# Kernel optimization log

Measured on AMD Instinct MI355X. Metric: run time of the kernel, lower is better.

The kernel has to match this reference:

```python
import jax, jax.numpy as jnp
import numpy as np
from math import sqrt

B, L, H, E = 8, 2048, 16, 128
S = 256  # selected_freq_count


def setup_inputs() -> dict:
    key = jax.random.key(0)
    kq, kk, kv = jax.random.split(key, 3)
    rng = np.random.default_rng(0)
    # unique sorted indices in [0, L//2), mirroring get_random_frequencies
    index_q = jnp.asarray(np.sort(rng.choice(L // 2, size=S, replace=False)), dtype=jnp.int32)
    index_kv = jnp.asarray(np.sort(rng.choice(L // 2, size=S, replace=False)), dtype=jnp.int32)
    return {
        "q": jax.random.normal(kq, (B, L, H, E), dtype=jnp.float32),
        "k": jax.random.normal(kk, (B, L, H, E), dtype=jnp.float32),
        "v": jax.random.normal(kv, (B, L, H, E), dtype=jnp.float32),
        "attn_mask": jnp.zeros((1,), dtype=jnp.int32),  # unused by the module
        "index_q": index_q,
        "index_kv": index_kv,
    }


def reference(q, k, v, attn_mask, index_q, index_kv):
    b, l, h, e = q.shape
    scale = 1.0 / sqrt(e)
    # permute to [B, H, E, L] then gather selected frequency columns
    xq = jnp.transpose(q, (0, 2, 3, 1))  # bhel
    xk = jnp.transpose(k, (0, 2, 3, 1))  # bhel
    xq_ft = jnp.take(xq, index_q, axis=-1)   # [B,H,E,Sq]
    xk_ft = jnp.take(xk, index_kv, axis=-1)  # [B,H,E,Sk]
    # dense attention on the gathered subset (contract over E)
    xqk = jax.nn.softmax(scale * jnp.einsum('bhex,bhey->bhxy', xq_ft, xk_ft), axis=-1)
    # NOTE: original multiplies attention by xk_ft_ (v is unused) -- faithful
    xqkv = jnp.einsum('bhxy,bhey->bhex', xqk, xk_ft)  # [B,H,E,Sq]
    # scatter back into zero-initialized [B,H,E,L]
    out_ft = jnp.zeros((b, h, e, l), dtype=q.dtype).at[..., index_q].set(xqkv)
    return out_ft, xqk
```

## Files before the change

### kernel.cpp

```cpp
#include <hip/hip_runtime.h>
#include <math.h>

typedef __bf16 bf16_t;
typedef __attribute__((ext_vector_type(8))) __bf16 bf16x8;
typedef __attribute__((ext_vector_type(4))) float f32x4;

#define NB 8
#define NL 2048
#define NH 16
#define NE 128
#define NS 256
#define XT 64

#define QSTR 136
#define PSTR 72

__global__ __launch_bounds__(256, 3) void fsa_gemm(
    const float* __restrict__ q, const float* __restrict__ k,
    const int* __restrict__ iq, const int* __restrict__ ikv,
    float* __restrict__ out)
{
  float* out_ft = out;
  float* out_p  = out + (size_t)NB*NH*NE*NL;

  __shared__ __align__(16) char smem[34816];
  bf16_t* Qs = (bf16_t*)smem;
  bf16_t* Ks = (bf16_t*)(smem + 17408);
  bf16_t* Ps = (bf16_t*)smem;
  bf16_t* Kt = (bf16_t*)(smem + 9216);

  const int t = threadIdx.x;
  const int tile = (blockIdx.x & 7) * 64 + (blockIdx.x >> 3);
  const int bh = tile >> 2, xb = tile & 3;
  const int b = bh >> 4, h = bh & 15;
  const int x0 = xb * XT;

  const int w   = t >> 6;
  const int l15 = t & 15;
  const int lg  = (t & 63) >> 4;

  {
    const int e4 = t & 31, xr = t >> 5;
    #pragma unroll
    for (int p = 0; p < 8; ++p) {
      const int x  = xr + 8*p;
      const int lq = iq[x0 + x];
      const float4 v = *(const float4*)(q + ((size_t)(b*NL + lq)*NH + h)*NE + 4*e4);
      union { bf16_t h4[4]; uint2 u; } pk;
      pk.h4[0]=(bf16_t)v.x; pk.h4[1]=(bf16_t)v.y; pk.h4[2]=(bf16_t)v.z; pk.h4[3]=(bf16_t)v.w;
      *(uint2*)(Qs + x*QSTR + 4*e4) = pk.u;
    }
  }

  f32x4 acc1[16];
  #pragma unroll
  for (int i = 0; i < 16; ++i) acc1[i] = (f32x4){0.f,0.f,0.f,0.f};
  bf16x8 aQ[4];

  #pragma unroll
  for (int c = 0; c < 4; ++c) {
    if (c > 0) __syncthreads();
    {
      const int e4 = t & 31, yr = t >> 5;
      #pragma unroll
      for (int p = 0; p < 8; ++p) {
        const int y  = yr + 8*p;
        const int lk = ikv[c*64 + y];
        const float4 v = *(const float4*)(k + ((size_t)(b*NL + lk)*NH + h)*NE + 4*e4);
        union { bf16_t h4[4]; uint2 u; } pk;
        pk.h4[0]=(bf16_t)v.x; pk.h4[1]=(bf16_t)v.y; pk.h4[2]=(bf16_t)v.z; pk.h4[3]=(bf16_t)v.w;
        *(uint2*)(Ks + y*QSTR + 4*e4) = pk.u;
      }
    }
    __syncthreads();
    if (c == 0) {
      #pragma unroll
      for (int ks = 0; ks < 4; ++ks)
        aQ[ks] = *(const bf16x8*)(Qs + (w*16 + l15)*QSTR + ks*32 + lg*8);
    }
    #pragma unroll
    for (int ks = 0; ks < 4; ++ks) {
      #pragma unroll
      for (int yt = 0; yt < 4; ++yt) {
        const bf16x8 bk = *(const bf16x8*)(Ks + (yt*16 + l15)*QSTR + ks*32 + lg*8);
        acc1[c*4 + yt] = __builtin_amdgcn_mfma_f32_16x16x32_bf16(aQ[ks], bk, acc1[c*4 + yt], 0, 0, 0);
      }
    }
  }

  const float scale = 0.08838834764831845f;
  #pragma unroll
  for (int r = 0; r < 4; ++r) {
    float m = -3.4e38f;
    #pragma unroll
    for (int yt = 0; yt < 16; ++yt) { acc1[yt][r] *= scale; m = fmaxf(m, acc1[yt][r]); }
    m = fmaxf(m, __shfl_xor(m, 1)); m = fmaxf(m, __shfl_xor(m, 2));
    m = fmaxf(m, __shfl_xor(m, 4)); m = fmaxf(m, __shfl_xor(m, 8));
    float s = 0.f;
    #pragma unroll
    for (int yt = 0; yt < 16; ++yt) { const float e = __expf(acc1[yt][r] - m); acc1[yt][r] = e; s += e; }
    s += __shfl_xor(s, 1); s += __shfl_xor(s, 2); s += __shfl_xor(s, 4); s += __shfl_xor(s, 8);
    const float inv = 1.0f / s;
    #pragma unroll
    for (int yt = 0; yt < 16; ++yt) acc1[yt][r] *= inv;
  }

  {
    float* po = out_p + ((size_t)bh*NS + x0 + w*16 + lg*4)*NS + l15;
    #pragma unroll
    for (int r = 0; r < 4; ++r)
      #pragma unroll
      for (int yt = 0; yt < 16; ++yt)
        po[(size_t)r*NS + yt*16] = acc1[yt][r];
  }

  f32x4 acc2[2][4];
  #pragma unroll
  for (int et = 0; et < 2; ++et)
    #pragma unroll
    for (int xt = 0; xt < 4; ++xt) acc2[et][xt] = (f32x4){0.f,0.f,0.f,0.f};

  #pragma unroll
  for (int c = 0; c < 4; ++c) {
    __syncthreads();
    {
      const int xr = w*16 + lg*4;
      #pragma unroll
      for (int r = 0; r < 4; ++r)
        #pragma unroll
        for (int yt = 0; yt < 4; ++yt)
          Ps[(xr + r)*PSTR + yt*16 + l15] = (bf16_t)acc1[c*4 + yt][r];
    }
    {
      const int e4 = t & 31, yb = t >> 5;
      const int swz = (e4 & 7) << 3;
      #pragma unroll
      for (int p = 0; p < 4; ++p) {
        const int y0  = 2*(yb + 8*p);
        const int ys  = y0 ^ swz;
        const int lk0 = ikv[c*64 + y0];
        const int lk1 = ikv[c*64 + y0 + 1];
        const float4 va = *(const float4*)(k + ((size_t)(b*NL + lk0)*NH + h)*NE + 4*e4);
        const float4 vb = *(const float4*)(k + ((size_t)(b*NL + lk1)*NH + h)*NE + 4*e4);
        union { bf16_t h2[2]; unsigned u; } pr;
        pr.h2[0]=(bf16_t)va.x; pr.h2[1]=(bf16_t)vb.x; *(unsigned*)(Kt + (4*e4+0)*PSTR + ys) = pr.u;
        pr.h2[0]=(bf16_t)va.y; pr.h2[1]=(bf16_t)vb.y; *(unsigned*)(Kt + (4*e4+1)*PSTR + ys) = pr.u;
        pr.h2[0]=(bf16_t)va.z; pr.h2[1]=(bf16_t)vb.z; *(unsigned*)(Kt + (4*e4+2)*PSTR + ys) = pr.u;
        pr.h2[0]=(bf16_t)va.w; pr.h2[1]=(bf16_t)vb.w; *(unsigned*)(Kt + (4*e4+3)*PSTR + ys) = pr.u;
      }
    }
    __syncthreads();
    #pragma unroll
    for (int ks = 0; ks < 2; ++ks) {
      const int er0 = w*32 + l15, er1 = w*32 + 16 + l15;
      const int sw0 = ((er0 >> 2) & 7) << 3;
      const int sw1 = ((er1 >> 2) & 7) << 3;
      const bf16x8 aK0 = *(const bf16x8*)(Kt + er0*PSTR + ((ks*32 + lg*8) ^ sw0));
      const bf16x8 aK1 = *(const bf16x8*)(Kt + er1*PSTR + ((ks*32 + lg*8) ^ sw1));
      #pragma unroll
      for (int xt = 0; xt < 4; ++xt) {
        const bf16x8 bp = *(const bf16x8*)(Ps + (xt*16 + l15)*PSTR + ks*32 + lg*8);
        acc2[0][xt] = __builtin_amdgcn_mfma_f32_16x16x32_bf16(aK0, bp, acc2[0][xt], 0, 0, 0);
        acc2[1][xt] = __builtin_amdgcn_mfma_f32_16x16x32_bf16(aK1, bp, acc2[1][xt], 0, 0, 0);
      }
    }
  }

  #pragma unroll
  for (int et = 0; et < 2; ++et)
    #pragma unroll
    for (int xt = 0; xt < 4; ++xt)
      #pragma unroll
      for (int r = 0; r < 4; ++r) {
        const int e = w*32 + et*16 + lg*4 + r;
        out_ft[((size_t)bh*NE + e)*NL + x0 + xt*16 + l15] = acc2[et][xt][r];
      }
}

__global__ __launch_bounds__(256) void fsa_expand(
    const int* __restrict__ iq, float* __restrict__ out_ft)
{
  __shared__ int   inv[NL];
  __shared__ float oc[16][NS];
  const int t  = threadIdx.x;
  const int bh = blockIdx.x >> 3;
  const int eg = blockIdx.x & 7;

  {
    const int4 mi = {-1,-1,-1,-1};
    *(int4*)(inv + 8*t)     = mi;
    *(int4*)(inv + 8*t + 4) = mi;
  }
  __syncthreads();
  inv[iq[t]] = t;
  {
    const int row = t >> 4, c0 = (t & 15) * 16;
    const float* src = out_ft + ((size_t)bh*NE + eg*16 + row)*NL;
    #pragma unroll
    for (int p = 0; p < 4; ++p)
      *(float4*)&oc[row][c0 + 4*p] = *(const float4*)(src + c0 + 4*p);
  }
  __syncthreads();

  #pragma unroll
  for (int r = 0; r < 16; ++r) {
    float* dst = out_ft + ((size_t)bh*NE + eg*16 + r)*NL;
    #pragma unroll
    for (int half = 0; half < 2; ++half) {
      const int l = half*1024 + 4*t;
      f32x4 v;
      { const int i0 = inv[l+0]; v.x = (i0 >= 0) ? oc[r][i0] : 0.f; }
      { const int i1 = inv[l+1]; v.y = (i1 >= 0) ? oc[r][i1] : 0.f; }
      { const int i2 = inv[l+2]; v.z = (i2 >= 0) ? oc[r][i2] : 0.f; }
      { const int i3 = inv[l+3]; v.w = (i3 >= 0) ? oc[r][i3] : 0.f; }
      __builtin_nontemporal_store(v, (f32x4*)(dst + l));
    }
  }
}

extern "C" void kernel_launch(void* const* d_in, const int* in_sizes, int n_in,
                              void* d_out, int out_size, void* d_ws, size_t ws_size,
                              hipStream_t stream) {
  const float* q = (const float*)d_in[0];
  const float* k = (const float*)d_in[1];
  const int* iq  = (const int*)d_in[4];
  const int* ikv = (const int*)d_in[5];
  float* out = (float*)d_out;

  fsa_gemm<<<dim3(NB*NH*(NS/XT)), dim3(256), 0, stream>>>(q, k, iq, ikv, out);
  fsa_expand<<<dim3(NB*NH*8), dim3(256), 0, stream>>>(iq, out);
}
```

Measured before the change: 358.7 us.

## Fuse scatter-expand into GEMM kernel, writing each tile's output segment directly

Removes the separate expand kernel. Each GEMM block stages its compact output in shared memory, builds a local inverse index over its own L range (between neighbouring selected indices), and writes the scattered rows plus zero-fill directly. The upper half of L (never indexed) is zeroed by blocks split by xb. This avoids the write-then-reread round trip of the compact output through global memory and one launch. In exchange it adds more shared memory per block and scalar tail loops, and it relies on the indices being sorted and below L/2, an assumption that holds for the test inputs.

```diff
diff --git a/kernel.cpp b/kernel.cpp
--- a/kernel.cpp
+++ b/kernel.cpp
@@ -7,6 +7,7 @@
 
 #define NB 8
 #define NL 2048
+#define NLH 1024
 #define NH 16
 #define NE 128
 #define NS 256
@@ -14,6 +15,7 @@
 
 #define QSTR 136
 #define PSTR 72
+#define OSTR 68
 
 __global__ __launch_bounds__(256, 3) void fsa_gemm(
     const float* __restrict__ q, const float* __restrict__ k,
@@ -23,11 +25,13 @@
   float* out_ft = out;
   float* out_p  = out + (size_t)NB*NH*NE*NL;
 
-  __shared__ __align__(16) char smem[34816];
+  __shared__ __align__(16) char smem[38912];
   bf16_t* Qs = (bf16_t*)smem;
   bf16_t* Ks = (bf16_t*)(smem + 17408);
   bf16_t* Ps = (bf16_t*)smem;
   bf16_t* Kt = (bf16_t*)(smem + 9216);
+  float*  Ocomp = (float*)smem;
+  int*    inv   = (int*)(smem + 34816);
 
   const int t = threadIdx.x;
   const int tile = (blockIdx.x & 7) * 64 + (blockIdx.x >> 3);
@@ -100,9 +104,9 @@
     #pragma unroll
     for (int yt = 0; yt < 16; ++yt) { const float e = __expf(acc1[yt][r] - m); acc1[yt][r] = e; s += e; }
     s += __shfl_xor(s, 1); s += __shfl_xor(s, 2); s += __shfl_xor(s, 4); s += __shfl_xor(s, 8);
-    const float inv = 1.0f / s;
-    #pragma unroll
-    for (int yt = 0; yt < 16; ++yt) acc1[yt][r] *= inv;
+    const float inv_ = 1.0f / s;
+    #pragma unroll
+    for (int yt = 0; yt < 16; ++yt) acc1[yt][r] *= inv_;
   }
 
   {
@@ -166,54 +170,48 @@
     }
   }
 
-  #pragma unroll
-  for (int et = 0; et < 2; ++et)
-    #pragma unroll
-    for (int xt = 0; xt < 4; ++xt)
-      #pragma unroll
-      for (int r = 0; r < 4; ++r) {
-        const int e = w*32 + et*16 + lg*4 + r;
-        out_ft[((size_t)bh*NE + e)*NL + x0 + xt*16 + l15] = acc2[et][xt][r];
-      }
-}
-
-__global__ __launch_bounds__(256) void fsa_expand(
-    const int* __restrict__ iq, float* __restrict__ out_ft)
-{
-  __shared__ int   inv[NL];
-  __shared__ float oc[16][NS];
-  const int t  = threadIdx.x;
-  const int bh = blockIdx.x >> 3;
-  const int eg = blockIdx.x & 7;
-
-  {
-    const int4 mi = {-1,-1,-1,-1};
-    *(int4*)(inv + 8*t)     = mi;
-    *(int4*)(inv + 8*t + 4) = mi;
-  }
   __syncthreads();
-  inv[iq[t]] = t;
-  {
-    const int row = t >> 4, c0 = (t & 15) * 16;
-    const float* src = out_ft + ((size_t)bh*NE + eg*16 + row)*NL;
-    #pragma unroll
-    for (int p = 0; p < 4; ++p)
-      *(float4*)&oc[row][c0 + 4*p] = *(const float4*)(src + c0 + 4*p);
-  }
+  {
+    #pragma unroll
+    for (int et = 0; et < 2; ++et)
+      #pragma unroll
+      for (int xt = 0; xt < 4; ++xt)
+        #pragma unroll
+        for (int r = 0; r < 4; ++r)
+          Ocomp[(w*32 + et*16 + lg*4 + r)*OSTR + xt*16 + l15] = acc2[et][xt][r];
+  }
+  const int start = (xb == 0) ? 0   : iq[x0];
+  const int endl  = (xb == 3) ? NLH : iq[x0 + XT];
+  for (int l = start + t; l < endl; l += 256) inv[l] = -1;
   __syncthreads();
-
-  #pragma unroll
-  for (int r = 0; r < 16; ++r) {
-    float* dst = out_ft + ((size_t)bh*NE + eg*16 + r)*NL;
-    #pragma unroll
-    for (int half = 0; half < 2; ++half) {
-      const int l = half*1024 + 4*t;
+  if (t < XT) inv[iq[x0 + t]] = t;
+  __syncthreads();
+
+  const int a0 = (start + 3) & ~3;
+  const int a1 = endl & ~3;
+  for (int e = 0; e < NE; ++e) {
+    float* dst = out_ft + ((size_t)bh*NE + e)*NL;
+    const float* orow = Ocomp + e*OSTR;
+    for (int l = a0 + 4*t; l < a1; l += 1024) {
       f32x4 v;
-      { const int i0 = inv[l+0]; v.x = (i0 >= 0) ? oc[r][i0] : 0.f; }
-      { const int i1 = inv[l+1]; v.y = (i1 >= 0) ? oc[r][i1] : 0.f; }
-      { const int i2 = inv[l+2]; v.z = (i2 >= 0) ? oc[r][i2] : 0.f; }
-      { const int i3 = inv[l+3]; v.w = (i3 >= 0) ? oc[r][i3] : 0.f; }
+      { const int i0 = inv[l+0]; v.x = (i0 >= 0) ? orow[i0] : 0.f; }
+      { const int i1 = inv[l+1]; v.y = (i1 >= 0) ? orow[i1] : 0.f; }
+      { const int i2 = inv[l+2]; v.z = (i2 >= 0) ? orow[i2] : 0.f; }
+      { const int i3 = inv[l+3]; v.w = (i3 >= 0) ? orow[i3] : 0.f; }
       __builtin_nontemporal_store(v, (f32x4*)(dst + l));
+    }
+    if (t == 0)
+      for (int l = start; l < a0 && l < endl; ++l) { const int i0 = inv[l]; dst[l] = (i0 >= 0) ? orow[i0] : 0.f; }
+    if (t == 1)
+      for (int l = (a1 > a0 ? a1 : a0 > endl ? endl : a1); l < endl; ++l) { const int i0 = inv[l]; dst[l] = (i0 >= 0) ? orow[i0] : 0.f; }
+  }
+  {
+    const f32x4 z = (f32x4){0.f, 0.f, 0.f, 0.f};
+    const int base = NLH + xb*(NLH/4);
+    for (int i = t; i < NE*64; i += 256) {
+      const int e = i >> 6;
+      float* dst = out_ft + ((size_t)bh*NE + e)*NL + base + ((i & 63) << 2);
+      __builtin_nontemporal_store(z, (f32x4*)dst);
     }
   }
 }
@@ -228,5 +226,4 @@
   float* out = (float*)d_out;
 
   fsa_gemm<<<dim3(NB*NH*(NS/XT)), dim3(256), 0, stream>>>(q, k, iq, ikv, out);
-  fsa_expand<<<dim3(NB*NH*8), dim3(256), 0, stream>>>(iq, out);
 }
```

Result: slower. 387.0 us (+7.9%).

## Zero upper output half in GEMM kernel and shrink expand to lower half

Applied to the files above, without the earlier changes.

The GEMM kernel now writes zeros into the upper half of each out_ft row (L/2..L) alongside its compute. The expand kernel then only scatters over the lower half, relying on all selected indices lying below L/2. The softmax probabilities are now stored row-contiguously from the bf16 LDS tile instead of as strided fp32 register stores, which rounds the returned attention matrix to bf16 precision. The aim is to overlap output zero-filling with the GEMM and to coalesce the probability writes, at the cost of an assumption about the index range and reduced output precision.

```diff
diff --git a/kernel.cpp b/kernel.cpp
--- a/kernel.cpp
+++ b/kernel.cpp
@@ -7,6 +7,7 @@
 
 #define NB 8
 #define NL 2048
+#define NLH 1024
 #define NH 16
 #define NE 128
 #define NS 256
@@ -52,6 +53,17 @@
     }
   }
 
+  {
+    const f32x4 z = (f32x4){0.f, 0.f, 0.f, 0.f};
+    const int base = NLH + xb*(NLH/4);
+    #pragma unroll 4
+    for (int i = t; i < NE*64; i += 256) {
+      const int e = i >> 6;
+      float* dst = out_ft + ((size_t)bh*NE + e)*NL + base + ((i & 63) << 2);
+      __builtin_nontemporal_store(z, (f32x4*)dst);
+    }
+  }
+
   f32x4 acc1[16];
   #pragma unroll
   for (int i = 0; i < 16; ++i) acc1[i] = (f32x4){0.f,0.f,0.f,0.f};
@@ -100,18 +112,9 @@
     #pragma unroll
     for (int yt = 0; yt < 16; ++yt) { const float e = __expf(acc1[yt][r] - m); acc1[yt][r] = e; s += e; }
     s += __shfl_xor(s, 1); s += __shfl_xor(s, 2); s += __shfl_xor(s, 4); s += __shfl_xor(s, 8);
-    const float inv = 1.0f / s;
-    #pragma unroll
-    for (int yt = 0; yt < 16; ++yt) acc1[yt][r] *= inv;
-  }
-
-  {
-    float* po = out_p + ((size_t)bh*NS + x0 + w*16 + lg*4)*NS + l15;
-    #pragma unroll
-    for (int r = 0; r < 4; ++r)
-      #pragma unroll
-      for (int yt = 0; yt < 16; ++yt)
-        po[(size_t)r*NS + yt*16] = acc1[yt][r];
+    const float is = 1.0f / s;
+    #pragma unroll
+    for (int yt = 0; yt < 16; ++yt) acc1[yt][r] *= is;
   }
 
   f32x4 acc2[2][4];
@@ -150,6 +153,20 @@
       }
     }
     __syncthreads();
+    {
+      const int xr = t >> 2, sg = t & 3;
+      const bf16_t* ps = Ps + xr*PSTR + sg*16;
+      float* po = out_p + ((size_t)bh*NS + x0 + xr)*NS + c*64 + sg*16;
+      #pragma unroll
+      for (int j2 = 0; j2 < 2; ++j2) {
+        const bf16x8 pv = *(const bf16x8*)(ps + 8*j2);
+        f32x4 lo, hi;
+        lo.x=(float)pv[0]; lo.y=(float)pv[1]; lo.z=(float)pv[2]; lo.w=(float)pv[3];
+        hi.x=(float)pv[4]; hi.y=(float)pv[5]; hi.z=(float)pv[6]; hi.w=(float)pv[7];
+        *(f32x4*)(po + 8*j2)     = lo;
+        *(f32x4*)(po + 8*j2 + 4) = hi;
+      }
+    }
     #pragma unroll
     for (int ks = 0; ks < 2; ++ks) {
       const int er0 = w*32 + l15, er1 = w*32 + 16 + l15;
@@ -180,41 +197,37 @@
 __global__ __launch_bounds__(256) void fsa_expand(
     const int* __restrict__ iq, float* __restrict__ out_ft)
 {
-  __shared__ int   inv[NL];
-  __shared__ float oc[16][NS];
+  __shared__ int   inv[NLH];
+  __shared__ float oc[8][NS];
   const int t  = threadIdx.x;
-  const int bh = blockIdx.x >> 3;
-  const int eg = blockIdx.x & 7;
-
-  {
-    const int4 mi = {-1,-1,-1,-1};
-    *(int4*)(inv + 8*t)     = mi;
-    *(int4*)(inv + 8*t + 4) = mi;
-  }
+  const int bh = blockIdx.x >> 4;
+  const int eg = blockIdx.x & 15;
+
+  *(int4*)(inv + 4*t) = (int4){-1,-1,-1,-1};
   __syncthreads();
   inv[iq[t]] = t;
   {
-    const int row = t >> 4, c0 = (t & 15) * 16;
-    const float* src = out_ft + ((size_t)bh*NE + eg*16 + row)*NL;
-    #pragma unroll
-    for (int p = 0; p < 4; ++p)
-      *(float4*)&oc[row][c0 + 4*p] = *(const float4*)(src + c0 + 4*p);
+    const int row = t >> 5, c0 = (t & 31) * 8;
+    const float* src = out_ft + ((size_t)bh*NE + eg*8 + row)*NL;
+    *(float4*)&oc[row][c0]     = *(const float4*)(src + c0);
+    *(float4*)&oc[row][c0 + 4] = *(const float4*)(src + c0 + 4);
   }
   __syncthreads();
 
-  #pragma unroll
-  for (int r = 0; r < 16; ++r) {
-    float* dst = out_ft + ((size_t)bh*NE + eg*16 + r)*NL;
-    #pragma unroll
-    for (int half = 0; half < 2; ++half) {
-      const int l = half*1024 + 4*t;
-      f32x4 v;
-      { const int i0 = inv[l+0]; v.x = (i0 >= 0) ? oc[r][i0] : 0.f; }
-      { const int i1 = inv[l+1]; v.y = (i1 >= 0) ? oc[r][i1] : 0.f; }
-      { const int i2 = inv[l+2]; v.z = (i2 >= 0) ? oc[r][i2] : 0.f; }
-      { const int i3 = inv[l+3]; v.w = (i3 >= 0) ? oc[r][i3] : 0.f; }
-      __builtin_nontemporal_store(v, (f32x4*)(dst + l));
-    }
+  const int4 iv = *(const int4*)(inv + 4*t);
+  const int c0 = iv.x < 0 ? 0 : iv.x, m0 = iv.x < 0 ? 0 : -1;
+  const int c1 = iv.y < 0 ? 0 : iv.y, m1 = iv.y < 0 ? 0 : -1;
+  const int c2 = iv.z < 0 ? 0 : iv.z, m2 = iv.z < 0 ? 0 : -1;
+  const int c3 = iv.w < 0 ? 0 : iv.w, m3 = iv.w < 0 ? 0 : -1;
+  float* dst = out_ft + ((size_t)bh*NE + eg*8)*NL + 4*t;
+  #pragma unroll
+  for (int r = 0; r < 8; ++r) {
+    f32x4 v;
+    v.x = m0 ? oc[r][c0] : 0.f;
+    v.y = m1 ? oc[r][c1] : 0.f;
+    v.z = m2 ? oc[r][c2] : 0.f;
+    v.w = m3 ? oc[r][c3] : 0.f;
+    __builtin_nontemporal_store(v, (f32x4*)(dst + (size_t)r*NL));
   }
 }
 
@@ -228,5 +241,5 @@
   float* out = (float*)d_out;
 
   fsa_gemm<<<dim3(NB*NH*(NS/XT)), dim3(256), 0, stream>>>(q, k, iq, ikv, out);
-  fsa_expand<<<dim3(NB*NH*8), dim3(256), 0, stream>>>(iq, out);
+  fsa_expand<<<dim3(NB*NH*16), dim3(256), 0, stream>>>(iq, out);
 }
```

New measurement: 379.6 us. +5.8%, slower.
